# Performance work log

Measured on AMD Instinct MI355X. Metric: run time of the kernel, lower is better.

## Reference

```python
import jax, jax.numpy as jnp
import numpy as np

H = 128; TIME_DIM = 8; LAM = 0.01; NUM_LAYERS = 2; B = 64
N_FACT = 100000; N_COMP = 5000; E = 500000; D_FACT = 384; D_COMP = 64
MLP_IN = 2 + 2 * (TIME_DIM // 2) + 1  # 11


def setup_inputs() -> dict:
    key = jax.random.key(0)
    ks = jax.random.split(key, 40)
    rn = lambda k, sh, s=0.05: jax.random.normal(k, sh, jnp.float32) * s
    inp = {
        'x_fact': jax.random.normal(ks[0], (N_FACT, D_FACT), jnp.float32),
        'x_comp': jax.random.normal(ks[1], (N_COMP, D_COMP), jnp.float32),
        'ea_f2c': jax.random.uniform(ks[2], (E, 2), jnp.float32),
        'ea_c2f': jax.random.uniform(ks[3], (E, 2), jnp.float32),
        'ei_f2c_src': jax.random.randint(ks[4], (E,), 0, N_FACT, jnp.int32),
        'ei_f2c_dst': jax.random.randint(ks[5], (E,), 0, N_COMP, jnp.int32),
        'ei_c2f_src': jax.random.randint(ks[6], (E,), 0, N_COMP, jnp.int32),
        'ei_c2f_dst': jax.random.randint(ks[7], (E,), 0, N_FACT, jnp.int32),
        'fact_batch': jnp.sort(jax.random.randint(ks[8], (N_FACT,), 0, B, jnp.int32)),
        'comp_batch': jnp.sort(jax.random.randint(ks[9], (N_COMP,), 0, B, jnp.int32)),
        # lazy per-type input projections
        'W_in_fact': rn(ks[10], (D_FACT, H)), 'b_in_fact': jnp.zeros((H,), jnp.float32),
        'W_in_comp': rn(ks[11], (D_COMP, H)), 'b_in_comp': jnp.zeros((H,), jnp.float32),
        # EdgeAttrEncoder MLP: 11 -> 32 -> 16 -> 1
        'eW1': rn(ks[12], (MLP_IN, 32)), 'eb1': jnp.zeros((32,), jnp.float32),
        'eW2': rn(ks[13], (32, 16)), 'eb2': jnp.zeros((16,), jnp.float32),
        'eW3': rn(ks[14], (16, 1)), 'eb3': jnp.zeros((1,), jnp.float32),
        # GraphConv per layer (axis0) per edge type (axis1: 0=f->c, 1=c->f)
        'W_rel': rn(ks[15], (NUM_LAYERS, 2, H, H)), 'b_rel': jnp.zeros((NUM_LAYERS, 2, H), jnp.float32),
        'W_root': rn(ks[16], (NUM_LAYERS, 2, H, H)),
        # shared post LayerNorm per node type (axis0: 0=fact, 1=company)
        'ln_scale': jnp.ones((2, H), jnp.float32), 'ln_bias': jnp.zeros((2, H), jnp.float32),
        # classifier 2H -> H -> 1
        'Wc1': rn(ks[17], (2 * H, H)), 'bc1': jnp.zeros((H,), jnp.float32),
        'Wc2': rn(ks[18], (H, 1)), 'bc2': jnp.zeros((1,), jnp.float32),
    }
    return inp


def _edge_gate(ea, eW1, eb1, eW2, eb2, eW3, eb3):
    # ea: [E,2] -> gate [E]
    sent = jnp.clip(ea[:, 0:1], -1.0, 1.0)
    decay = ea[:, 1:2]
    # decay in [0,1] -> delta_t = -log(decay)/lambda, clamped >= 0
    dt = jnp.maximum(-jnp.log(jnp.clip(decay, 1e-6, None)) / LAM, 0.0)
    ds = jnp.clip(dt / 30.0, 0.0, 12.0)
    freqs = jnp.arange(1, TIME_DIM // 2 + 1, dtype=ds.dtype)
    tvec = jnp.concatenate([jnp.sin(ds * freqs), jnp.cos(ds * freqs), ds], axis=-1)
    x = jnp.concatenate([sent, jnp.log1p(dt), tvec], axis=-1)  # [E,11]
    h = jax.nn.relu(x @ eW1 + eb1)
    h = jax.nn.relu(h @ eW2 + eb2)
    return jax.nn.sigmoid(h @ eW3 + eb3)[:, 0]


def _layernorm(x, scale, bias, eps=1e-5):
    mu = jnp.mean(x, axis=-1, keepdims=True)
    var = jnp.var(x, axis=-1, keepdims=True)
    return (x - mu) * jax.lax.rsqrt(var + eps) * scale + bias


def _seg_mean(x, seg, n):
    s = jax.ops.segment_sum(x, seg, num_segments=n)
    c = jax.ops.segment_sum(jnp.ones((x.shape[0], 1), x.dtype), seg, num_segments=n)
    return s / jnp.maximum(c, 1.0)


def reference(x_fact, x_comp, ea_f2c, ea_c2f, ei_f2c_src, ei_f2c_dst, ei_c2f_src,
              ei_c2f_dst, fact_batch, comp_batch, W_in_fact, b_in_fact, W_in_comp,
              b_in_comp, eW1, eb1, eW2, eb2, eW3, eb3, W_rel, b_rel, W_root,
              ln_scale, ln_bias, Wc1, bc1, Wc2, bc2):
    # per-type input projection + ReLU
    xf = jax.nn.relu(x_fact @ W_in_fact + b_in_fact)   # [N_fact, H]
    xc = jax.nn.relu(x_comp @ W_in_comp + b_in_comp)   # [N_comp, H]
    # MLP-gated edge weights (shared encoder across relations)
    w_f2c = _edge_gate(ea_f2c, eW1, eb1, eW2, eb2, eW3, eb3)  # [E]
    w_c2f = _edge_gate(ea_c2f, eW1, eb1, eW2, eb2, eW3, eb3)  # [E]
    nf, nc = xf.shape[0], xc.shape[0]
    for l in range(NUM_LAYERS):
        prev_f, prev_c = xf, xc
        # GraphConv: lin_rel(sum_j w_ij * x_j) + lin_root(x_i)  (aggr='add')
        agg_c = jax.ops.segment_sum(xf[ei_f2c_src] * w_f2c[:, None], ei_f2c_dst, num_segments=nc)
        new_c = agg_c @ W_rel[l, 0] + b_rel[l, 0] + xc @ W_root[l, 0]
        agg_f = jax.ops.segment_sum(xc[ei_c2f_src] * w_c2f[:, None], ei_c2f_dst, num_segments=nf)
        new_f = agg_f @ W_rel[l, 1] + b_rel[l, 1] + xf @ W_root[l, 1]
        # ReLU -> residual -> shared per-type LayerNorm
        xf = _layernorm(jax.nn.relu(new_f) + prev_f, ln_scale[0], ln_bias[0])
        xc = _layernorm(jax.nn.relu(new_c) + prev_c, ln_scale[1], ln_bias[1])
    fact_pool = _seg_mean(xf, fact_batch, B)   # [B, H]
    comp_pool = _seg_mean(xc, comp_batch, B)   # [B, H]
    pooled = jnp.concatenate([fact_pool, comp_pool], axis=-1)  # [B, 2H]
    h = jax.nn.relu(pooled @ Wc1 + bc1)
    return (h @ Wc2 + bc2)[:, 0]  # [B] logits
```

## Files before the change

kernel.cpp:

```cpp
#include <hip/hip_runtime.h>
#include <math.h>

#define H 128
#define EDGES 500000
#define NFACT 100000
#define NCOMP 5000
#define BATCH 64
#define NTILE 6250

typedef _Float16 half8_t __attribute__((ext_vector_type(8)));
typedef float floatx4 __attribute__((ext_vector_type(4)));

__device__ inline short4 f4_to_h4(float4 v){
  union { short4 s; _Float16 h[4]; } u;
  u.h[0]=(_Float16)v.x; u.h[1]=(_Float16)v.y; u.h[2]=(_Float16)v.z; u.h[3]=(_Float16)v.w;
  return u.s;
}

__device__ inline half8_t f8_to_h8(float4 a, float4 b){
  half8_t r;
  r[0]=(_Float16)a.x; r[1]=(_Float16)a.y; r[2]=(_Float16)a.z; r[3]=(_Float16)a.w;
  r[4]=(_Float16)b.x; r[5]=(_Float16)b.y; r[6]=(_Float16)b.z; r[7]=(_Float16)b.w;
  return r;
}

__global__ void k_hist(const int* __restrict__ dst, int n, int* __restrict__ cnt){
  for (int e = blockIdx.x*blockDim.x + threadIdx.x; e < n; e += gridDim.x*blockDim.x)
    atomicAdd(&cnt[dst[e]], 1);
}

__global__ __launch_bounds__(1024) void k_scan1(const int* __restrict__ cnt, int n,
                                                int* __restrict__ offs, int* __restrict__ part){
  __shared__ int sh[1024];
  int tid = threadIdx.x;
  int i = blockIdx.x*1024 + tid;
  int v = (i < n) ? cnt[i] : 0;
  sh[tid] = v;
  __syncthreads();
  for (int d = 1; d < 1024; d <<= 1){
    int t = (tid >= d) ? sh[tid-d] : 0;
    __syncthreads();
    sh[tid] += t;
    __syncthreads();
  }
  if (i < n) offs[i] = sh[tid] - v;
  if (tid == 1023) part[blockIdx.x] = sh[1023];
}

__global__ void k_scan2(int* part, int nb){
  __shared__ int sh[128];
  int tid = threadIdx.x;
  int v = (tid < nb) ? part[tid] : 0;
  sh[tid] = v;
  __syncthreads();
  for (int d = 1; d < 128; d <<= 1){
    int t = (tid >= d) ? sh[tid-d] : 0;
    __syncthreads();
    sh[tid] += t;
    __syncthreads();
  }
  if (tid < nb) part[tid] = sh[tid] - v;
}

__global__ __launch_bounds__(1024) void k_scan3(int* offs, int n, const int* __restrict__ part, int total){
  int i = blockIdx.x*1024 + threadIdx.x;
  if (i < n) offs[i] += part[blockIdx.x];
  if (i == 0) offs[n] = total;
}

__global__ void k_fill2(const int* __restrict__ src, const int* __restrict__ dst,
                        const float* __restrict__ w, int n, const int* __restrict__ offs,
                        int* __restrict__ cur, int4* __restrict__ ed){
  for (int e = blockIdx.x*blockDim.x + threadIdx.x; e < n; e += gridDim.x*blockDim.x){
    int d = dst[e];
    int p = offs[d] + atomicAdd(&cur[d], 1);
    ed[p] = make_int4(src[e], __float_as_int(w[e]), d, 0);
  }
}

__global__ __launch_bounds__(256) void k_prep(const float* __restrict__ W_in,
                                              const float* __restrict__ W_rel,
                                              const float* __restrict__ W_root,
                                              _Float16* __restrict__ wt_in,
                                              _Float16* __restrict__ wcat0,
                                              _Float16* __restrict__ wcat1){
  int i = blockIdx.x*256 + threadIdx.x;
  if (i < 49152){
    int n = i / 384, k = i % 384;
    wt_in[i] = (_Float16)W_in[k*128 + n];
  } else if (i < 49152 + 32768){
    int j = i - 49152;
    int n = j / 256, k = j % 256;
    const float* Wr = W_rel  + 1*16384;
    const float* Wo = W_root + 1*16384;
    wcat0[j] = (_Float16)(k < 128 ? Wr[k*128+n] : Wo[(k-128)*128+n]);
  } else if (i < 49152 + 65536){
    int j = i - 49152 - 32768;
    int n = j / 256, k = j % 256;
    const float* Wr = W_rel  + 3*16384;
    const float* Wo = W_root + 3*16384;
    wcat1[j] = (_Float16)(k < 128 ? Wr[k*128+n] : Wo[(k-128)*128+n]);
  }
}

__global__ __launch_bounds__(256) void k_gate(const float* __restrict__ ea,
                       const float* __restrict__ eW1, const float* __restrict__ eb1,
                       const float* __restrict__ eW2, const float* __restrict__ eb2,
                       const float* __restrict__ eW3, const float* __restrict__ eb3,
                       float* __restrict__ wout, int n){
  __shared__ float w1[11*32], b1[32], w2[32*16], b2[16], w3[16];
  __shared__ float b3;
  int tid = threadIdx.x;
  for (int i = tid; i < 11*32; i += blockDim.x) w1[i] = eW1[i];
  for (int i = tid; i < 32;    i += blockDim.x) b1[i] = eb1[i];
  for (int i = tid; i < 32*16; i += blockDim.x) w2[i] = eW2[i];
  for (int i = tid; i < 16;    i += blockDim.x) b2[i] = eb2[i];
  for (int i = tid; i < 16;    i += blockDim.x) w3[i] = eW3[i];
  if (tid == 0) b3 = eb3[0];
  __syncthreads();
  for (int e = blockIdx.x*blockDim.x + tid; e < n; e += gridDim.x*blockDim.x){
    float2 eav = ((const float2*)ea)[e];
    float sent  = fminf(fmaxf(eav.x, -1.f), 1.f);
    float decay = eav.y;
    float dt = fmaxf(-logf(fmaxf(decay, 1e-6f)) * 100.f, 0.f);
    float ds = fminf(dt * (1.f/30.f), 12.f);
    float s1 = sinf(ds), c1 = cosf(ds);
    float s2v = 2.f*s1*c1;
    float c2v = 1.f - 2.f*s1*s1;
    float s3v = s1*c2v + c1*s2v;
    float c3v = c1*c2v - s1*s2v;
    float s4v = 2.f*s2v*c2v;
    float c4v = 1.f - 2.f*s2v*s2v;
    float x[11];
    x[0] = sent; x[1] = log1pf(dt);
    x[2] = s1;  x[3] = s2v; x[4] = s3v; x[5] = s4v;
    x[6] = c1;  x[7] = c2v; x[8] = c3v; x[9] = c4v;
    x[10] = ds;
    float s2[16];
    #pragma unroll
    for (int j = 0; j < 16; j++) s2[j] = b2[j];
    #pragma unroll
    for (int i = 0; i < 32; i++){
      float h = b1[i];
      #pragma unroll
      for (int k = 0; k < 11; k++) h += x[k]*w1[k*32+i];
      h = fmaxf(h, 0.f);
      #pragma unroll
      for (int j = 0; j < 16; j++) s2[j] += h*w2[i*16+j];
    }
    float o = b3;
    #pragma unroll
    for (int j = 0; j < 16; j++) o += fmaxf(s2[j], 0.f)*w3[j];
    wout[e] = 1.f/(1.f + expf(-o));
  }
}

template<int K, int R>
__global__ __launch_bounds__(128) void k_input_s(const float* __restrict__ X, const float* __restrict__ W,
                                                 const float* __restrict__ bias, float* __restrict__ Y){
  __shared__ float xs[R*K];
  int t = threadIdx.x;
  long row0 = (long)blockIdx.x * R;
  const float4* src = (const float4*)(X + row0*K);
  float4* d4 = (float4*)xs;
  for (int i = t; i < R*K/4; i += 128) d4[i] = src[i];
  __syncthreads();
  float acc[R];
  #pragma unroll
  for (int r = 0; r < R; r++) acc[r] = 0.f;
  for (int k4 = 0; k4 < K/4; k4++){
    int kb = k4*4;
    float w0 = W[(kb+0)*H+t], w1 = W[(kb+1)*H+t], w2 = W[(kb+2)*H+t], w3 = W[(kb+3)*H+t];
    #pragma unroll
    for (int r = 0; r < R; r++){
      float4 xv = ((const float4*)(xs + r*K))[k4];
      acc[r] += xv.x*w0 + xv.y*w1 + xv.z*w2 + xv.w*w3;
    }
  }
  float b = bias[t];
  #pragma unroll
  for (int r = 0; r < R; r++)
    Y[(row0+r)*H + t] = fmaxf(acc[r] + b, 0.f);
}

__global__ __launch_bounds__(256, 2) void k_input_m(const float* __restrict__ X,
                                                 const _Float16* __restrict__ Wt,
                                                 const float* __restrict__ bias,
                                                 float* __restrict__ Y){
  __shared__ _Float16 xs[16][392];
  int t = threadIdx.x;
  int lane = t & 63, wv = t >> 6;
  int m = lane & 15, q = lane >> 4;

  half8_t wreg[2][12];
  float bcol[2];
  #pragma unroll
  for (int j = 0; j < 2; j++){
    int col = (wv*2 + j)*16 + m;
    const _Float16* wb = Wt + (size_t)col*384 + q*8;
    #pragma unroll
    for (int ks = 0; ks < 12; ks++) wreg[j][ks] = *(const half8_t*)(wb + ks*32);
    bcol[j] = bias[col];
  }

  int row_i[6], c4_i[6];
  #pragma unroll
  for (int i = 0; i < 6; i++){
    int idx = i*256 + t;
    row_i[i] = idx/96; c4_i[i] = idx - row_i[i]*96;
  }

  int tpb = (NTILE + gridDim.x - 1)/gridDim.x;
  int tb0 = blockIdx.x*tpb, tb1 = tb0 + tpb;
  if (tb1 > NTILE) tb1 = NTILE;
  if (tb0 >= tb1) return;

  const float4* X4 = (const float4*)X;
  float4 r[6];
  #pragma unroll
  for (int i = 0; i < 6; i++) r[i] = X4[(size_t)tb0*1536 + i*256 + t];

  for (int tile = tb0; tile < tb1; ++tile){
    __syncthreads();
    #pragma unroll
    for (int i = 0; i < 6; i++)
      *(short4*)&xs[row_i[i]][c4_i[i]*4] = f4_to_h4(r[i]);
    __syncthreads();
    if (tile + 1 < tb1){
      size_t base = (size_t)(tile+1)*1536;
      #pragma unroll
      for (int i = 0; i < 6; i++) r[i] = X4[base + i*256 + t];
    }
    __builtin_amdgcn_sched_barrier(0);

    floatx4 acc0 = (floatx4){0.f,0.f,0.f,0.f};
    floatx4 acc1 = (floatx4){0.f,0.f,0.f,0.f};
    #pragma unroll
    for (int ks = 0; ks < 12; ks++){
      half8_t av = *(const half8_t*)&xs[m][ks*32 + q*8];
      acc0 = __builtin_amdgcn_mfma_f32_16x16x32_f16(av, wreg[0][ks], acc0, 0, 0, 0);
      acc1 = __builtin_amdgcn_mfma_f32_16x16x32_f16(av, wreg[1][ks], acc1, 0, 0, 0);
    }
    long rb = (long)tile*16;
    #pragma unroll
    for (int j = 0; j < 2; j++){
      floatx4 a = j ? acc1 : acc0;
      int col = (wv*2 + j)*16 + m;
      #pragma unroll
      for (int i2 = 0; i2 < 4; i2++)
        Y[(rb + q*4 + i2)*H + col] = fmaxf(a[i2] + bcol[j], 0.f);
    }
  }
}

__global__ __launch_bounds__(64) void k_layer_m(
    const float* __restrict__ xsrc, const float* __restrict__ xprev,
    const int* __restrict__ offs, const int4* __restrict__ ed,
    const _Float16* __restrict__ Wt, const float* __restrict__ brel,
    const float* __restrict__ lnsc, const float* __restrict__ lnbi,
    float* __restrict__ xnext){
  __shared__ _Float16 xin[16][264];
  int t = threadIdx.x, c = t & 31, g = t >> 5;
  long row0 = (long)blockIdx.x * 16;
  int grow0 = g*8;
  #pragma unroll
  for (int j = 0; j < 8; j++){
    int lr = grow0 + j;
    ((short4*)&xin[lr][0])[c] = make_short4(0,0,0,0);
    float4 pv = ((const float4*)(xprev + (row0+lr)*H))[c];
    ((short4*)&xin[lr][128])[c] = f4_to_h4(pv);
  }
  int lo = offs[row0 + grow0], hi = offs[row0 + grow0 + 8];
  float4 a = make_float4(0.f,0.f,0.f,0.f);
  int cur = (int)row0 + grow0;
  int idx = lo;
  for (; idx + 8 <= hi; idx += 8){
    int4 mrec[8];
    #pragma unroll
    for (int j = 0; j < 8; j++) mrec[j] = ed[idx+j];
    float4 v[8];
    #pragma unroll
    for (int j = 0; j < 8; j++) v[j] = ((const float4*)(xsrc + (long)mrec[j].x*H))[c];
    #pragma unroll
    for (int j = 0; j < 8; j++){
      float w = __int_as_float(mrec[j].y);
      if (mrec[j].z != cur){ ((short4*)&xin[cur-(int)row0][0])[c] = f4_to_h4(a); a = make_float4(0.f,0.f,0.f,0.f); cur = mrec[j].z; }
      a.x += v[j].x*w; a.y += v[j].y*w; a.z += v[j].z*w; a.w += v[j].w*w;
    }
  }
  for (; idx < hi; idx++){
    int4 mrec = ed[idx];
    float4 v = ((const float4*)(xsrc + (long)mrec.x*H))[c];
    float w = __int_as_float(mrec.y);
    if (mrec.z != cur){ ((short4*)&xin[cur-(int)row0][0])[c] = f4_to_h4(a); a = make_float4(0.f,0.f,0.f,0.f); cur = mrec.z; }
    a.x += v.x*w; a.y += v.y*w; a.z += v.z*w; a.w += v.w*w;
  }
  if (lo < hi) ((short4*)&xin[cur-(int)row0][0])[c] = f4_to_h4(a);

  int m = t & 15, q = t >> 4;
  floatx4 acc[8];
  #pragma unroll
  for (int nt = 0; nt < 8; nt++) acc[nt] = (floatx4){0.f,0.f,0.f,0.f};
  #pragma unroll
  for (int ks = 0; ks < 8; ks++){
    half8_t av = *(const half8_t*)&xin[m][ks*32 + q*8];
    #pragma unroll
    for (int nt = 0; nt < 8; nt++){
      half8_t bv = *(const half8_t*)(Wt + (size_t)(nt*16 + m)*256 + ks*32 + q*8);
      acc[nt] = __builtin_amdgcn_mfma_f32_16x16x32_f16(av, bv, acc[nt], 0, 0, 0);
    }
  }
  float vs[8][4];
  float s[4] = {0.f,0.f,0.f,0.f}, ss[4] = {0.f,0.f,0.f,0.f};
  #pragma unroll
  for (int nt = 0; nt < 8; nt++){
    int col = nt*16 + m;
    float b = brel[col];
    #pragma unroll
    for (int i = 0; i < 4; i++){
      int lr = q*4 + i;
      float pv = (float)xin[lr][128 + col];
      float v = fmaxf(acc[nt][i] + b, 0.f) + pv;
      vs[nt][i] = v;
      s[i] += v; ss[i] += v*v;
    }
  }
  #pragma unroll
  for (int i = 0; i < 4; i++){
    #pragma unroll
    for (int mm = 1; mm < 16; mm <<= 1){
      s[i]  += __shfl_xor(s[i],  mm, 64);
      ss[i] += __shfl_xor(ss[i], mm, 64);
    }
  }
  #pragma unroll
  for (int nt = 0; nt < 8; nt++){
    int col = nt*16 + m;
    float lsc = lnsc[col], lbi = lnbi[col];
    #pragma unroll
    for (int i = 0; i < 4; i++){
      float mu  = s[i]*(1.f/H);
      float var = ss[i]*(1.f/H) - mu*mu;
      float rstd = rsqrtf(var + 1e-5f);
      xnext[(row0 + q*4 + i)*H + col] = (vs[nt][i] - mu)*rstd*lsc + lbi;
    }
  }
}

template<int R>
__global__ __launch_bounds__(128) void k_layer(
    const float* __restrict__ xsrc, const float* __restrict__ xprev,
    const int* __restrict__ offs, const int4* __restrict__ ed,
    const float* __restrict__ Wrel, const float* __restrict__ brel,
    const float* __restrict__ Wroot, const float* __restrict__ lnsc,
    const float* __restrict__ lnbi, float* __restrict__ xnext){
  constexpr int RG = R/4;
  __shared__ float xin[R][256];
  int t = threadIdx.x, c = t & 31, g = t >> 5;
  long row0 = (long)blockIdx.x * R;
  int grow0 = g*RG;
  #pragma unroll
  for (int j = 0; j < RG; j++){
    int lr = grow0 + j;
    ((float4*)&xin[lr][0])[c] = make_float4(0.f,0.f,0.f,0.f);
    ((float4*)&xin[lr][128])[c] = ((const float4*)(xprev + (row0+lr)*H))[c];
  }
  int lo = offs[row0 + grow0], hi = offs[row0 + grow0 + RG];
  float4 a = make_float4(0.f,0.f,0.f,0.f);
  int cur = (int)row0 + grow0;
  int idx = lo;
  for (; idx + 8 <= hi; idx += 8){
    int4 m[8];
    #pragma unroll
    for (int j = 0; j < 8; j++) m[j] = ed[idx+j];
    float4 v[8];
    #pragma unroll
    for (int j = 0; j < 8; j++) v[j] = ((const float4*)(xsrc + (long)m[j].x*H))[c];
    #pragma unroll
    for (int j = 0; j < 8; j++){
      float w = __int_as_float(m[j].y);
      if (m[j].z != cur){ ((float4*)&xin[cur-(int)row0][0])[c] = a; a = make_float4(0.f,0.f,0.f,0.f); cur = m[j].z; }
      a.x += v[j].x*w; a.y += v[j].y*w; a.z += v[j].z*w; a.w += v[j].w*w;
    }
  }
  for (; idx < hi; idx++){
    int4 m = ed[idx];
    float4 v = ((const float4*)(xsrc + (long)m.x*H))[c];
    float w = __int_as_float(m.y);
    if (m.z != cur){ ((float4*)&xin[cur-(int)row0][0])[c] = a; a = make_float4(0.f,0.f,0.f,0.f); cur = m.z; }
    a.x += v.x*w; a.y += v.y*w; a.z += v.z*w; a.w += v.w*w;
  }
  if (lo < hi) ((float4*)&xin[cur-(int)row0][0])[c] = a;

  float4 acc[RG];
  float4 bv = ((const float4*)brel)[c];
  #pragma unroll
  for (int j = 0; j < RG; j++) acc[j] = bv;
  #pragma unroll
  for (int p = 0; p < 2; p++){
    const float4* Wp = (const float4*)(p ? Wroot : Wrel) + c;
    #pragma unroll 4
    for (int k4 = 0; k4 < 32; k4++){
      float4 xv[RG];
      #pragma unroll
      for (int j = 0; j < RG; j++)
        xv[j] = ((const float4*)xin[grow0+j])[p*32 + k4];
      #pragma unroll
      for (int kk = 0; kk < 4; kk++){
        float4 wv = Wp[(size_t)(k4*4+kk)*32];
        #pragma unroll
        for (int j = 0; j < RG; j++){
          float xk = (kk==0) ? xv[j].x : (kk==1) ? xv[j].y : (kk==2) ? xv[j].z : xv[j].w;
          acc[j].x += xk*wv.x; acc[j].y += xk*wv.y; acc[j].z += xk*wv.z; acc[j].w += xk*wv.w;
        }
      }
    }
  }
  float4 lsc = ((const float4*)lnsc)[c];
  float4 lbi = ((const float4*)lnbi)[c];
  #pragma unroll
  for (int j = 0; j < RG; j++){
    int lr = grow0 + j;
    float4 pv = ((const float4*)&xin[lr][128])[c];
    float4 v;
    v.x = fmaxf(acc[j].x, 0.f) + pv.x;
    v.y = fmaxf(acc[j].y, 0.f) + pv.y;
    v.z = fmaxf(acc[j].z, 0.f) + pv.z;
    v.w = fmaxf(acc[j].w, 0.f) + pv.w;
    float s  = v.x + v.y + v.z + v.w;
    float ss = v.x*v.x + v.y*v.y + v.z*v.z + v.w*v.w;
    #pragma unroll
    for (int mm = 1; mm < 32; mm <<= 1){ s += __shfl_xor(s, mm, 64); ss += __shfl_xor(ss, mm, 64); }
    float mu  = s*(1.f/H);
    float var = ss*(1.f/H) - mu*mu;
    float rstd = rsqrtf(var + 1e-5f);
    float4 o;
    o.x = (v.x - mu)*rstd*lsc.x + lbi.x;
    o.y = (v.y - mu)*rstd*lsc.y + lbi.y;
    o.z = (v.z - mu)*rstd*lsc.z + lbi.z;
    o.w = (v.w - mu)*rstd*lsc.w + lbi.w;
    ((float4*)(xnext + (row0+lr)*H))[c] = o;
  }
}

#define PCHUNK 128
#define FBLK ((NFACT + PCHUNK - 1) / PCHUNK)
#define CBLK ((NCOMP + PCHUNK - 1) / PCHUNK)

__global__ __launch_bounds__(128) void k_pool_acc(const float* __restrict__ xf, const float* __restrict__ xc,
                                                  const int* __restrict__ fb, const int* __restrict__ cb,
                                                  float* __restrict__ pooled){
  int t = threadIdx.x;
  int b = blockIdx.x;
  if (b < FBLK){
    int start = b*PCHUNK, end = start + PCHUNK; if (end > NFACT) end = NFACT;
    float s = 0.f; int curb = -1;
    for (int i = start; i < end; i++){
      int bb = fb[i];
      if (bb != curb){
        if (curb >= 0) atomicAdd(&pooled[curb*256 + t], s);
        curb = bb; s = 0.f;
      }
      s += xf[(long)i*H + t];
    }
    if (curb >= 0) atomicAdd(&pooled[curb*256 + t], s);
  } else {
    int bbk = b - FBLK;
    int start = bbk*PCHUNK, end = start + PCHUNK; if (end > NCOMP) end = NCOMP;
    float s = 0.f; int curb = -1;
    for (int i = start; i < end; i++){
      int bb = cb[i];
      if (bb != curb){
        if (curb >= 0) atomicAdd(&pooled[curb*256 + 128 + t], s);
        curb = bb; s = 0.f;
      }
      s += xc[(long)i*H + t];
    }
    if (curb >= 0) atomicAdd(&pooled[curb*256 + 128 + t], s);
  }
}

__device__ inline int lowerb(const int* a, int n, int key){
  int lo = 0, hi = n;
  while (lo < hi){ int m = (lo+hi) >> 1; if (a[m] < key) lo = m+1; else hi = m; }
  return lo;
}

__global__ __launch_bounds__(128) void k_head(const float* __restrict__ pooled,
                                              const int* __restrict__ fb, const int* __restrict__ cb,
                                              const float* __restrict__ Wc1, const float* __restrict__ bc1,
                                              const float* __restrict__ Wc2, const float* __restrict__ bc2,
                                              float* __restrict__ out){
  __shared__ float p[256];
  __shared__ float red[2];
  int t = threadIdx.x, b = blockIdx.x;
  int flo = lowerb(fb, NFACT, b), fhi = lowerb(fb, NFACT, b+1);
  int clo = lowerb(cb, NCOMP, b), chi = lowerb(cb, NCOMP, b+1);
  float fc = (float)((fhi - flo) > 1 ? (fhi - flo) : 1);
  float cc = (float)((chi - clo) > 1 ? (chi - clo) : 1);
  p[t]       = pooled[b*256 + t] / fc;
  p[128 + t] = pooled[b*256 + 128 + t] / cc;
  __syncthreads();
  float acc = bc1[t];
  #pragma unroll 4
  for (int k = 0; k < 256; k++) acc += p[k]*Wc1[k*H + t];
  float h = fmaxf(acc, 0.f)*Wc2[t];
  #pragma unroll
  for (int m = 1; m < 64; m <<= 1) h += __shfl_xor(h, m, 64);
  if ((t & 63) == 0) red[t>>6] = h;
  __syncthreads();
  if (t == 0) out[b] = red[0] + red[1] + bc2[0];
}

extern "C" void kernel_launch(void* const* d_in, const int* in_sizes, int n_in,
                              void* d_out, int out_size, void* d_ws, size_t ws_size,
                              hipStream_t stream){
  const float* x_fact = (const float*)d_in[0];
  const float* x_comp = (const float*)d_in[1];
  const float* ea_f2c = (const float*)d_in[2];
  const float* ea_c2f = (const float*)d_in[3];
  const int* s_f2c   = (const int*)d_in[4];
  const int* dst_f2c = (const int*)d_in[5];
  const int* s_c2f   = (const int*)d_in[6];
  const int* dst_c2f = (const int*)d_in[7];
  const int* fb = (const int*)d_in[8];
  const int* cb = (const int*)d_in[9];
  const float* W_in_f = (const float*)d_in[10];
  const float* b_in_f = (const float*)d_in[11];
  const float* W_in_c = (const float*)d_in[12];
  const float* b_in_c = (const float*)d_in[13];
  const float* eW1 = (const float*)d_in[14]; const float* eb1 = (const float*)d_in[15];
  const float* eW2 = (const float*)d_in[16]; const float* eb2 = (const float*)d_in[17];
  const float* eW3 = (const float*)d_in[18]; const float* eb3 = (const float*)d_in[19];
  const float* W_rel = (const float*)d_in[20]; const float* b_rel = (const float*)d_in[21];
  const float* W_root = (const float*)d_in[22];
  const float* ln_s = (const float*)d_in[23]; const float* ln_b = (const float*)d_in[24];
  const float* Wc1 = (const float*)d_in[25]; const float* bc1 = (const float*)d_in[26];
  const float* Wc2 = (const float*)d_in[27]; const float* bc2 = (const float*)d_in[28];
  float* out = (float*)d_out;

  char* ws = (char*)d_ws;
  size_t off = 0;
  auto alloc = [&](size_t bytes)->char*{ char* p = ws + off; off = (off + bytes + 255) & ~(size_t)255; return p; };
  float* xf0   = (float*)alloc((size_t)NFACT*H*4);
  float* xf1   = (float*)alloc((size_t)NFACT*H*4);
  float* xc0   = (float*)alloc((size_t)NCOMP*H*4);
  float* xc1   = (float*)alloc((size_t)NCOMP*H*4);
  float* w_f2c = (float*)alloc((size_t)EDGES*4);
  float* w_c2f = (float*)alloc((size_t)EDGES*4);
  int4* ed_f2c = (int4*)alloc((size_t)EDGES*16);
  int4* ed_c2f = (int4*)alloc((size_t)EDGES*16);
  int* off_f2c = (int*)alloc((size_t)(NCOMP+1)*4);
  int* cur_f2c = (int*)alloc((size_t)NCOMP*4);
  int* off_c2f = (int*)alloc((size_t)(NFACT+1)*4);
  int* cur_c2f = (int*)alloc((size_t)NFACT*4);
  int* part    = (int*)alloc(128*4);
  float* pooled= (float*)alloc((size_t)BATCH*256*4);
  _Float16* wt_in = (_Float16*)alloc((size_t)49152*2);
  _Float16* wcat0 = (_Float16*)alloc((size_t)32768*2);
  _Float16* wcat1 = (_Float16*)alloc((size_t)32768*2);

  k_prep<<<448,256,0,stream>>>(W_in_f, W_rel, W_root, wt_in, wcat0, wcat1);
  k_gate<<<512,256,0,stream>>>(ea_f2c, eW1,eb1,eW2,eb2,eW3,eb3, w_f2c, EDGES);
  k_gate<<<512,256,0,stream>>>(ea_c2f, eW1,eb1,eW2,eb2,eW3,eb3, w_c2f, EDGES);

  hipMemsetAsync(cur_f2c, 0, NCOMP*4, stream);
  k_hist<<<512,256,0,stream>>>(dst_f2c, EDGES, cur_f2c);
  {
    int nb = (NCOMP + 1023)/1024;
    k_scan1<<<nb,1024,0,stream>>>(cur_f2c, NCOMP, off_f2c, part);
    k_scan2<<<1,128,0,stream>>>(part, nb);
    k_scan3<<<nb,1024,0,stream>>>(off_f2c, NCOMP, part, EDGES);
  }
  hipMemsetAsync(cur_f2c, 0, NCOMP*4, stream);
  k_fill2<<<512,256,0,stream>>>(s_f2c, dst_f2c, w_f2c, EDGES, off_f2c, cur_f2c, ed_f2c);

  hipMemsetAsync(cur_c2f, 0, NFACT*4, stream);
  k_hist<<<512,256,0,stream>>>(dst_c2f, EDGES, cur_c2f);
  {
    int nb = (NFACT + 1023)/1024;
    k_scan1<<<nb,1024,0,stream>>>(cur_c2f, NFACT, off_c2f, part);
    k_scan2<<<1,128,0,stream>>>(part, nb);
    k_scan3<<<nb,1024,0,stream>>>(off_c2f, NFACT, part, EDGES);
  }
  hipMemsetAsync(cur_c2f, 0, NFACT*4, stream);
  k_fill2<<<512,256,0,stream>>>(s_c2f, dst_c2f, w_c2f, EDGES, off_c2f, cur_c2f, ed_c2f);

  k_input_m<<<512,256,0,stream>>>(x_fact, wt_in, b_in_f, xf0);
  k_input_s<64,8><<<NCOMP/8,128,0,stream>>>(x_comp, W_in_c, b_in_c, xc0);

  const float* xf_p = xf0; const float* xc_p = xc0;
  float* xf_n = xf1; float* xc_n = xc1;
  for (int l = 0; l < 2; l++){
    const float* Wr0 = W_rel  + (size_t)(l*2+0)*H*H;
    const float* br0 = b_rel  + (size_t)(l*2+0)*H;
    const float* br1 = b_rel  + (size_t)(l*2+1)*H;
    const float* Wo0 = W_root + (size_t)(l*2+0)*H*H;
    const _Float16* wcat = (l == 0) ? wcat0 : wcat1;
    k_layer<4><<<NCOMP/4,128,0,stream>>>(xf_p, xc_p, off_f2c, ed_f2c,
                                         Wr0, br0, Wo0, ln_s + H, ln_b + H, xc_n);
    k_layer_m<<<NFACT/16,64,0,stream>>>(xc_p, xf_p, off_c2f, ed_c2f,
                                        wcat, br1, ln_s, ln_b, xf_n);
    const float* tf = xf_p; xf_p = xf_n; xf_n = (float*)tf;
    const float* tc = xc_p; xc_p = xc_n; xc_n = (float*)tc;
  }

  hipMemsetAsync(pooled, 0, (size_t)BATCH*256*4, stream);
  k_pool_acc<<<FBLK + CBLK,128,0,stream>>>(xf_p, xc_p, fb, cb, pooled);
  k_head<<<BATCH,128,0,stream>>>(pooled, fb, cb, Wc1, bc1, Wc2, bc2, out);
}
```

Measured before the change: 919.9 us.

## Fuse gate and histogram kernels, merge CSR fills, stage output stores via LDS

Merges the two edge-gate launches into one kernel that also performs the destination histogram atomics, which removes the separate histogram kernels. The two CSR fill kernels are merged into one launch covering both edge directions. The input-projection and fact-layer kernels now stage their outputs through shared memory so each row is written with coalesced float4 stores instead of scattered scalar stores. This costs extra shared memory and a synchronization per tile, and the gate kernel gains atomics on its critical path.

Result: faster. 885.8 us (-3.7%).

```diff
diff --git a/kernel.cpp b/kernel.cpp
--- a/kernel.cpp
+++ b/kernel.cpp
@@ -15,18 +15,6 @@
   union { short4 s; _Float16 h[4]; } u;
   u.h[0]=(_Float16)v.x; u.h[1]=(_Float16)v.y; u.h[2]=(_Float16)v.z; u.h[3]=(_Float16)v.w;
   return u.s;
-}
-
-__device__ inline half8_t f8_to_h8(float4 a, float4 b){
-  half8_t r;
-  r[0]=(_Float16)a.x; r[1]=(_Float16)a.y; r[2]=(_Float16)a.z; r[3]=(_Float16)a.w;
-  r[4]=(_Float16)b.x; r[5]=(_Float16)b.y; r[6]=(_Float16)b.z; r[7]=(_Float16)b.w;
-  return r;
-}
-
-__global__ void k_hist(const int* __restrict__ dst, int n, int* __restrict__ cnt){
-  for (int e = blockIdx.x*blockDim.x + threadIdx.x; e < n; e += gridDim.x*blockDim.x)
-    atomicAdd(&cnt[dst[e]], 1);
 }
 
 __global__ __launch_bounds__(1024) void k_scan1(const int* __restrict__ cnt, int n,
@@ -68,13 +56,25 @@
   if (i == 0) offs[n] = total;
 }
 
-__global__ void k_fill2(const int* __restrict__ src, const int* __restrict__ dst,
-                        const float* __restrict__ w, int n, const int* __restrict__ offs,
-                        int* __restrict__ cur, int4* __restrict__ ed){
-  for (int e = blockIdx.x*blockDim.x + threadIdx.x; e < n; e += gridDim.x*blockDim.x){
-    int d = dst[e];
-    int p = offs[d] + atomicAdd(&cur[d], 1);
-    ed[p] = make_int4(src[e], __float_as_int(w[e]), d, 0);
+__global__ void k_fill2d(const int* __restrict__ src0, const int* __restrict__ dst0,
+                         const float* __restrict__ w0, const int* __restrict__ offs0,
+                         int* __restrict__ cur0, int4* __restrict__ ed0,
+                         const int* __restrict__ src1, const int* __restrict__ dst1,
+                         const float* __restrict__ w1, const int* __restrict__ offs1,
+                         int* __restrict__ cur1, int4* __restrict__ ed1, int n){
+  int total = 2*n;
+  for (int idx = blockIdx.x*blockDim.x + threadIdx.x; idx < total; idx += gridDim.x*blockDim.x){
+    if (idx < n){
+      int e = idx;
+      int d = dst0[e];
+      int p = offs0[d] + atomicAdd(&cur0[d], 1);
+      ed0[p] = make_int4(src0[e], __float_as_int(w0[e]), d, 0);
+    } else {
+      int e = idx - n;
+      int d = dst1[e];
+      int p = offs1[d] + atomicAdd(&cur1[d], 1);
+      ed1[p] = make_int4(src1[e], __float_as_int(w1[e]), d, 0);
+    }
   }
 }
 
@@ -103,11 +103,14 @@
   }
 }
 
-__global__ __launch_bounds__(256) void k_gate(const float* __restrict__ ea,
+__global__ __launch_bounds__(256) void k_gate2(const float* __restrict__ ea0,
+                       const float* __restrict__ ea1,
+                       const int* __restrict__ dst0, const int* __restrict__ dst1,
+                       int* __restrict__ cnt0, int* __restrict__ cnt1,
                        const float* __restrict__ eW1, const float* __restrict__ eb1,
                        const float* __restrict__ eW2, const float* __restrict__ eb2,
                        const float* __restrict__ eW3, const float* __restrict__ eb3,
-                       float* __restrict__ wout, int n){
+                       float* __restrict__ wout0, float* __restrict__ wout1, int n){
   __shared__ float w1[11*32], b1[32], w2[32*16], b2[16], w3[16];
   __shared__ float b3;
   int tid = threadIdx.x;
@@ -118,8 +121,11 @@
   for (int i = tid; i < 16;    i += blockDim.x) w3[i] = eW3[i];
   if (tid == 0) b3 = eb3[0];
   __syncthreads();
-  for (int e = blockIdx.x*blockDim.x + tid; e < n; e += gridDim.x*blockDim.x){
-    float2 eav = ((const float2*)ea)[e];
+  int total = 2*n;
+  for (int idx = blockIdx.x*blockDim.x + tid; idx < total; idx += gridDim.x*blockDim.x){
+    int dir = idx >= n;
+    int e = dir ? idx - n : idx;
+    float2 eav = dir ? ((const float2*)ea1)[e] : ((const float2*)ea0)[e];
     float sent  = fminf(fmaxf(eav.x, -1.f), 1.f);
     float decay = eav.y;
     float dt = fmaxf(-logf(fmaxf(decay, 1e-6f)) * 100.f, 0.f);
@@ -151,7 +157,9 @@
     float o = b3;
     #pragma unroll
     for (int j = 0; j < 16; j++) o += fmaxf(s2[j], 0.f)*w3[j];
-    wout[e] = 1.f/(1.f + expf(-o));
+    float wv = 1.f/(1.f + expf(-o));
+    if (dir){ wout1[e] = wv; atomicAdd(&cnt1[dst1[e]], 1); }
+    else    { wout0[e] = wv; atomicAdd(&cnt0[dst0[e]], 1); }
   }
 }
 
@@ -188,6 +196,7 @@
                                                  const float* __restrict__ bias,
                                                  float* __restrict__ Y){
   __shared__ _Float16 xs[16][392];
+  __shared__ float tb[4*16*36];
   int t = threadIdx.x;
   int lane = t & 63, wv = t >> 6;
   int m = lane & 15, q = lane >> 4;
@@ -219,6 +228,9 @@
   float4 r[6];
   #pragma unroll
   for (int i = 0; i < 6; i++) r[i] = X4[(size_t)tb0*1536 + i*256 + t];
+
+  float* tbw = &tb[wv*576];
+  int rowl = lane >> 2, c8l = lane & 3;
 
   for (int tile = tb0; tile < tb1; ++tile){
     __syncthreads();
@@ -245,10 +257,17 @@
     #pragma unroll
     for (int j = 0; j < 2; j++){
       floatx4 a = j ? acc1 : acc0;
-      int col = (wv*2 + j)*16 + m;
+      int lc = j*16 + m;
       #pragma unroll
       for (int i2 = 0; i2 < 4; i2++)
-        Y[(rb + q*4 + i2)*H + col] = fmaxf(a[i2] + bcol[j], 0.f);
+        tbw[(q*4+i2)*36 + lc] = fmaxf(a[i2] + bcol[j], 0.f);
+    }
+    __syncthreads();
+    {
+      const float* srcp = tbw + rowl*36 + c8l*8;
+      float* dstp = Y + (rb + rowl)*H + wv*32 + c8l*8;
+      *(float4*)dstp       = *(const float4*)(srcp);
+      *(float4*)(dstp + 4) = *(const float4*)(srcp + 4);
     }
   }
 }
@@ -260,6 +279,7 @@
     const float* __restrict__ lnsc, const float* __restrict__ lnbi,
     float* __restrict__ xnext){
   __shared__ _Float16 xin[16][264];
+  __shared__ float tb[16*144];
   int t = threadIdx.x, c = t & 31, g = t >> 5;
   long row0 = (long)blockIdx.x * 16;
   int grow0 = g*8;
@@ -337,13 +357,23 @@
   for (int nt = 0; nt < 8; nt++){
     int col = nt*16 + m;
     float lsc = lnsc[col], lbi = lnbi[col];
+    int chnk = col >> 5, lc = col & 31;
     #pragma unroll
     for (int i = 0; i < 4; i++){
       float mu  = s[i]*(1.f/H);
       float var = ss[i]*(1.f/H) - mu*mu;
       float rstd = rsqrtf(var + 1e-5f);
-      xnext[(row0 + q*4 + i)*H + col] = (vs[nt][i] - mu)*rstd*lsc + lbi;
-    }
+      tb[(q*4+i)*144 + chnk*36 + lc] = (vs[nt][i] - mu)*rstd*lsc + lbi;
+    }
+  }
+  __syncthreads();
+  {
+    int rowl = t >> 2, c8 = t & 3;
+    const float* srcp = &tb[rowl*144 + c8*36];
+    float4* dst4 = (float4*)(xnext + (row0 + rowl)*H + c8*32);
+    #pragma unroll
+    for (int k = 0; k < 8; k++)
+      dst4[k] = *(const float4*)(srcp + k*4);
   }
 }
 
@@ -561,30 +591,28 @@
   _Float16* wcat1 = (_Float16*)alloc((size_t)32768*2);
 
   k_prep<<<448,256,0,stream>>>(W_in_f, W_rel, W_root, wt_in, wcat0, wcat1);
-  k_gate<<<512,256,0,stream>>>(ea_f2c, eW1,eb1,eW2,eb2,eW3,eb3, w_f2c, EDGES);
-  k_gate<<<512,256,0,stream>>>(ea_c2f, eW1,eb1,eW2,eb2,eW3,eb3, w_c2f, EDGES);
-
   hipMemsetAsync(cur_f2c, 0, NCOMP*4, stream);
-  k_hist<<<512,256,0,stream>>>(dst_f2c, EDGES, cur_f2c);
+  hipMemsetAsync(cur_c2f, 0, NFACT*4, stream);
+  k_gate2<<<1024,256,0,stream>>>(ea_f2c, ea_c2f, dst_f2c, dst_c2f,
+                                 cur_f2c, cur_c2f,
+                                 eW1,eb1,eW2,eb2,eW3,eb3, w_f2c, w_c2f, EDGES);
+
   {
     int nb = (NCOMP + 1023)/1024;
     k_scan1<<<nb,1024,0,stream>>>(cur_f2c, NCOMP, off_f2c, part);
     k_scan2<<<1,128,0,stream>>>(part, nb);
     k_scan3<<<nb,1024,0,stream>>>(off_f2c, NCOMP, part, EDGES);
   }
-  hipMemsetAsync(cur_f2c, 0, NCOMP*4, stream);
-  k_fill2<<<512,256,0,stream>>>(s_f2c, dst_f2c, w_f2c, EDGES, off_f2c, cur_f2c, ed_f2c);
-
-  hipMemsetAsync(cur_c2f, 0, NFACT*4, stream);
-  k_hist<<<512,256,0,stream>>>(dst_c2f, EDGES, cur_c2f);
   {
     int nb = (NFACT + 1023)/1024;
     k_scan1<<<nb,1024,0,stream>>>(cur_c2f, NFACT, off_c2f, part);
     k_scan2<<<1,128,0,stream>>>(part, nb);
     k_scan3<<<nb,1024,0,stream>>>(off_c2f, NFACT, part, EDGES);
   }
+  hipMemsetAsync(cur_f2c, 0, NCOMP*4, stream);
   hipMemsetAsync(cur_c2f, 0, NFACT*4, stream);
-  k_fill2<<<512,256,0,stream>>>(s_c2f, dst_c2f, w_c2f, EDGES, off_c2f, cur_c2f, ed_c2f);
+  k_fill2d<<<1024,256,0,stream>>>(s_f2c, dst_f2c, w_f2c, off_f2c, cur_f2c, ed_f2c,
+                                  s_c2f, dst_c2f, w_c2f, off_c2f, cur_c2f, ed_c2f, EDGES);
 
   k_input_m<<<512,256,0,stream>>>(x_fact, wt_in, b_in_f, xf0);
   k_input_s<64,8><<<NCOMP/8,128,0,stream>>>(x_comp, W_in_c, b_in_c, xc0);
```
